# Performance work log

Hardware: AMD Instinct MI355X
Metric: run time of the kernel (lower is better)

The kernel has to match this reference:

```python
import jax, jax.numpy as jnp
import numpy as np
import math

D_MODEL = 2048
N_HEADS = 16
HEAD_DIM = D_MODEL // N_HEADS  # 128
SEQ = 2048
BATCH = 1


def make_freqs(seq_len, head_dim, theta=10000.0):
    # standard rotary frequencies: freqs_cis = exp(i * t * inv_freq)
    inv_freq = 1.0 / (theta ** (np.arange(0, head_dim, 2, dtype=np.float32) / head_dim))
    t = np.arange(seq_len, dtype=np.float32)
    ang = np.outer(t, inv_freq)  # [seq, head_dim/2]
    return jnp.asarray(np.cos(ang)), jnp.asarray(np.sin(ang))


def setup_inputs() -> dict:
    key = jax.random.key(0)
    ks = jax.random.split(key, 6)
    x = jax.random.normal(ks[0], (BATCH, SEQ, D_MODEL), dtype=jnp.float32)
    freqs_cos, freqs_sin = make_freqs(SEQ, HEAD_DIM)
    # causal additive mask, broadcastable to [b, h, s, s]
    mask = jnp.where(jnp.tril(jnp.ones((SEQ, SEQ), dtype=bool)), 0.0, -1e9).astype(jnp.float32)[None, None]
    scale = 0.02
    wq = jax.random.normal(ks[1], (D_MODEL, D_MODEL), dtype=jnp.float32) * scale
    wk = jax.random.normal(ks[2], (D_MODEL, D_MODEL), dtype=jnp.float32) * scale
    wv = jax.random.normal(ks[3], (D_MODEL, D_MODEL), dtype=jnp.float32) * scale
    wo = jax.random.normal(ks[4], (D_MODEL, D_MODEL), dtype=jnp.float32) * scale
    return {"x": x, "freqs_cos": freqs_cos, "freqs_sin": freqs_sin, "mask": mask,
            "wq": wq, "wk": wk, "wv": wv, "wo": wo}


def _apply_rotary(q, k, cos, sin):
    # q, k: [b, s, h, hd]; cos/sin: [s, hd/2]
    def rot(t):
        tr = t.reshape(*t.shape[:-1], -1, 2)  # [b, s, h, hd/2, 2]
        re, im = tr[..., 0], tr[..., 1]
        c = cos[None, :, None, :]
        s = sin[None, :, None, :]
        # complex multiply (re + i im) * (c + i s)
        out_re = re * c - im * s
        out_im = re * s + im * c
        return jnp.stack([out_re, out_im], axis=-1).reshape(t.shape)
    return rot(q), rot(k)


def reference(x, freqs_cos, freqs_sin, mask, wq, wk, wv, wo):
    b, s, _ = x.shape
    # QKV projections (nn.Linear with no bias: x @ W^T; W is square so use x @ W
    # with W stored already-transposed -- weights here are random so x @ W is faithful math)
    q = (x @ wq).reshape(b, s, N_HEADS, HEAD_DIM)
    k = (x @ wk).reshape(b, s, N_HEADS, HEAD_DIM)
    v = (x @ wv).reshape(b, s, N_HEADS, HEAD_DIM)
    q, k = _apply_rotary(q, k, freqs_cos, freqs_sin)
    # [b, h, s_q, s_k]
    scores = jnp.einsum("bqhd,bkhd->bhqk", q, k) / math.sqrt(HEAD_DIM)
    scores = scores + mask
    probs = jax.nn.softmax(scores.astype(jnp.float32), axis=-1).astype(q.dtype)
    out = jnp.einsum("bhqk,bkhd->bqhd", probs, v).reshape(b, s, N_HEADS * HEAD_DIM)
    return out @ wo
```

## Files before the change

### kernel.cpp

```cpp
#include <hip/hip_runtime.h>
#include <hip/hip_bf16.h>
#include <math.h>

#define SEQ 2048
#define DM 2048
#define NH 16
#define HD 128
#define QKV_N 6144

typedef __bf16 bf16;
typedef __bf16 bf16x8 __attribute__((ext_vector_type(8)));
typedef __bf16 bf16x4v __attribute__((ext_vector_type(4)));
typedef __bf16 bf16x2v __attribute__((ext_vector_type(2)));
typedef float f32x4 __attribute__((ext_vector_type(4)));

__device__ inline int sw_idx64(int row, int chunk) {
    return (row * 8 + (chunk ^ (row & 7))) * 8;
}
__device__ inline int sw_idx128(int row, int chunk) {
    return (row * 16 + (chunk ^ (row & 15))) * 8;
}

__device__ inline void async16(const void* g, void* l) {
    __builtin_amdgcn_global_load_lds((const __attribute__((address_space(1))) void*)g,
                                     (__attribute__((address_space(3))) void*)l, 16, 0, 0);
}

__global__ __launch_bounds__(256) void k_prep(const float* __restrict__ wq,
                                              const float* __restrict__ wk,
                                              const float* __restrict__ wv,
                                              const float* __restrict__ wo,
                                              bf16* __restrict__ wT, bf16* __restrict__ woT,
                                              const float* __restrict__ x,
                                              bf16* __restrict__ xb) {
    const int z = blockIdx.z;
    const int t = threadIdx.x;
    if (z == 4) {
        int bid = blockIdx.y * 32 + blockIdx.x;
#pragma unroll
        for (int j = 0; j < 4; ++j) {
            int i = bid * 1024 + j * 256 + t;
            float4 v = ((const float4*)x)[i];
            bf16x4v o;
            o.x = (bf16)v.x; o.y = (bf16)v.y; o.z = (bf16)v.z; o.w = (bf16)v.w;
            ((bf16x4v*)xb)[i] = o;
        }
        return;
    }
    __shared__ bf16 tile[64][66];
    const float* src = (z == 0) ? wq : (z == 1) ? wk : (z == 2) ? wv : wo;
    bf16* dst = (z < 3) ? (wT + (size_t)z * DM * DM) : woT;
    const int bx = blockIdx.x * 64, by = blockIdx.y * 64;
#pragma unroll
    for (int j = 0; j < 4; ++j) {
        int idx = j * 256 + t;
        int r = idx >> 4, cg = idx & 15;
        float4 v = *(const float4*)&src[(size_t)(by + r) * DM + bx + cg * 4];
        bf16x4v o;
        o.x = (bf16)v.x; o.y = (bf16)v.y; o.z = (bf16)v.z; o.w = (bf16)v.w;
        *(bf16x4v*)&tile[r][cg * 4] = o;
    }
    __syncthreads();
#pragma unroll
    for (int j = 0; j < 4; ++j) {
        int idx = j * 256 + t;
        int r = idx >> 4, cg = idx & 15;
        bf16x4v o;
        o.x = tile[cg * 4 + 0][r];
        o.y = tile[cg * 4 + 1][r];
        o.z = tile[cg * 4 + 2][r];
        o.w = tile[cg * 4 + 3][r];
        *(bf16x4v*)&dst[(size_t)(bx + r) * DM + by + cg * 4] = o;
    }
}

__global__ __launch_bounds__(1024) void k_rope(bf16* __restrict__ qkv,
                                               const float* __restrict__ cosT,
                                               const float* __restrict__ sinT) {
    int idx = blockIdx.x * 1024 + threadIdx.x;
    int i = idx & 63;
    int h = (idx >> 6) & 15;
    int s = idx >> 10;
    float c = cosT[s * 64 + i], sn = sinT[s * 64 + i];
    size_t base = (size_t)s * QKV_N + h * HD + 2 * i;
    bf16x2v q = *(bf16x2v*)&qkv[base];
    float qr = (float)q.x, qi = (float)q.y;
    bf16x2v qo;
    qo.x = (bf16)(qr * c - qi * sn);
    qo.y = (bf16)(qr * sn + qi * c);
    *(bf16x2v*)&qkv[base] = qo;
    bf16x2v k = *(bf16x2v*)&qkv[base + DM];
    float kr = (float)k.x, ki = (float)k.y;
    bf16x2v ko;
    ko.x = (bf16)(kr * c - ki * sn);
    ko.y = (bf16)(kr * sn + ki * c);
    *(bf16x2v*)&qkv[base + DM] = ko;
}

__global__ __launch_bounds__(256) void k_vt(const bf16* __restrict__ qkv,
                                            bf16* __restrict__ vT) {
    __shared__ bf16 tile[64][66];
    const int t = threadIdx.x;
    const int bx = blockIdx.x * 64, by = blockIdx.y * 64;
#pragma unroll
    for (int j = 0; j < 4; ++j) {
        int idx = j * 256 + t;
        int r = idx >> 4, cg = idx & 15;
        *(bf16x4v*)&tile[r][cg * 4] =
            *(const bf16x4v*)&qkv[(size_t)(by + r) * QKV_N + 2 * DM + bx + cg * 4];
    }
    __syncthreads();
#pragma unroll
    for (int j = 0; j < 4; ++j) {
        int idx = j * 256 + t;
        int r = idx >> 4, cg = idx & 15;
        bf16x4v o;
        o.x = tile[cg * 4 + 0][r];
        o.y = tile[cg * 4 + 1][r];
        o.z = tile[cg * 4 + 2][r];
        o.w = tile[cg * 4 + 3][r];
        *(bf16x4v*)&vT[(size_t)(bx + r) * SEQ + by + cg * 4] = o;
    }
}

template <typename OutT, int BN>
__device__ __forceinline__ void gemm_body(const bf16* __restrict__ A,
                                          const bf16* __restrict__ Bt,
                                          OutT* __restrict__ C,
                                          int N, int K, size_t bm, size_t bn,
                                          bf16* As, bf16* Bs) {
    constexpr int NI = BN / 32;
    const int t = threadIdx.x;
    const int lane = t & 63;
    const int w = t >> 6;
    const int wr = (w >> 1) * 64, wc = (w & 1) * (BN / 2);
    const int l15 = lane & 15, quad = lane >> 4;
    f32x4 acc[4][NI];
#pragma unroll
    for (int i = 0; i < 4; ++i)
#pragma unroll
        for (int j = 0; j < NI; ++j) acc[i][j] = (f32x4){0.f, 0.f, 0.f, 0.f};

    for (int kt = 0; kt < K; kt += 64) {
#pragma unroll
        for (int j = 0; j < 4; ++j) {
            int c = j * 256 + t;
            int row = c >> 3, g = ((c & 7) ^ (row & 7)) * 8;
            async16(&A[(bm + row) * K + kt + g], &As[c * 8]);
        }
#pragma unroll
        for (int j = 0; j < NI; ++j) {
            int c = j * 256 + t;
            int row = c >> 3, g = ((c & 7) ^ (row & 7)) * 8;
            async16(&Bt[(bn + row) * K + kt + g], &Bs[c * 8]);
        }
        __syncthreads();
#pragma unroll
        for (int kh = 0; kh < 2; ++kh) {
            bf16x8 af[4], bfm[NI];
#pragma unroll
            for (int mi = 0; mi < 4; ++mi)
                af[mi] = *(const bf16x8*)&As[sw_idx64(wr + mi * 16 + l15, kh * 4 + quad)];
#pragma unroll
            for (int ni = 0; ni < NI; ++ni)
                bfm[ni] = *(const bf16x8*)&Bs[sw_idx64(wc + ni * 16 + l15, kh * 4 + quad)];
#pragma unroll
            for (int mi = 0; mi < 4; ++mi)
#pragma unroll
                for (int ni = 0; ni < NI; ++ni)
                    acc[mi][ni] = __builtin_amdgcn_mfma_f32_16x16x32_bf16(
                        af[mi], bfm[ni], acc[mi][ni], 0, 0, 0);
        }
        __syncthreads();
    }
#pragma unroll
    for (int mi = 0; mi < 4; ++mi)
#pragma unroll
        for (int ni = 0; ni < NI; ++ni)
#pragma unroll
            for (int r = 0; r < 4; ++r) {
                size_t row = bm + wr + mi * 16 + quad * 4 + r;
                size_t col = bn + wc + ni * 16 + l15;
                C[row * (size_t)N + col] = (OutT)acc[mi][ni][r];
            }
}

template <typename OutT, int BN>
__global__ __launch_bounds__(256) void k_gemm_bt(const bf16* __restrict__ A,
                                                 const bf16* __restrict__ Bt,
                                                 OutT* __restrict__ C,
                                                 int M, int N, int K) {
    __shared__ bf16 As[128 * 64];
    __shared__ bf16 Bs[BN * 64];
    size_t bm = (size_t)blockIdx.y * 128, bn = (size_t)blockIdx.x * BN;
    gemm_body<OutT, BN>(A, Bt, C, N, K, bm, bn, As, Bs);
}

__global__ __launch_bounds__(256) void k_flash(const bf16* __restrict__ qkv,
                                               const bf16* __restrict__ vT,
                                               bf16* __restrict__ out) {
    __shared__ bf16 Ks[2][64 * 128];
    __shared__ bf16 Vs[2][128 * 64];
    __shared__ bf16 Pl[4][16 * 64];
    const int t = threadIdx.x;
    const int lane = t & 63;
    const int w = t >> 6;
    const int l15 = lane & 15, quad = lane >> 4;
    const int b = blockIdx.x;
    const int h = (b & 7) * 2 + ((b >> 3) & 1);
    const int qb = 31 - (b >> 4);
    const int q0w = qb * 64 + w * 16;
    const float sc2 = 0.08838834764831845f * 1.4426950408889634f;

    const size_t qrow = (size_t)(q0w + l15) * QKV_N + h * HD;
    bf16x8 aq[4];
#pragma unroll
    for (int u = 0; u < 4; ++u)
        aq[u] = *(const bf16x8*)&qkv[qrow + u * 32 + quad * 8];

    f32x4 o[8];
#pragma unroll
    for (int c = 0; c < 8; ++c) o[c] = (f32x4){0.f, 0.f, 0.f, 0.f};
    float l_r[4] = {0.f, 0.f, 0.f, 0.f};

    int krow[4], kg[4], vrow[4], vg[4];
#pragma unroll
    for (int j = 0; j < 4; ++j) {
        int c = j * 256 + t;
        krow[j] = c >> 4; kg[j] = ((c & 15) ^ (krow[j] & 15)) * 8;
        vrow[j] = c >> 3; vg[j] = ((c & 7) ^ (vrow[j] & 7)) * 8;
    }
    auto stage = [&](int buf, int kt2) {
        const int kb2 = kt2 * 64;
#pragma unroll
        for (int j = 0; j < 4; ++j)
            async16(&qkv[(size_t)(kb2 + krow[j]) * QKV_N + DM + h * HD + kg[j]],
                    &Ks[buf][(j * 256 + t) * 8]);
#pragma unroll
        for (int j = 0; j < 4; ++j)
            async16(&vT[(size_t)(h * HD + vrow[j]) * SEQ + kb2 + vg[j]],
                    &Vs[buf][(j * 256 + t) * 8]);
    };

    const int n64 = qb + 1;
    stage(0, 0);
    for (int kt = 0; kt < n64; ++kt) {
        const int cb = kt & 1;
        const int kbase = kt * 64;
        if (kt + 1 < n64) {
            stage(cb ^ 1, kt + 1);
            asm volatile("s_waitcnt vmcnt(8)" ::: "memory");
        } else {
            asm volatile("s_waitcnt vmcnt(0)" ::: "memory");
        }
        __builtin_amdgcn_s_barrier();
        asm volatile("" ::: "memory");

        f32x4 s4[4];
#pragma unroll
        for (int sub = 0; sub < 4; ++sub) {
            f32x4 z = (f32x4){0.f, 0.f, 0.f, 0.f};
#pragma unroll
            for (int u = 0; u < 4; ++u) {
                bf16x8 kv = *(const bf16x8*)&Ks[cb][sw_idx128(sub * 16 + l15, u * 4 + quad)];
                z = __builtin_amdgcn_mfma_f32_16x16x32_bf16(aq[u], kv, z, 0, 0, 0);
            }
            s4[sub] = z;
        }
        const bool masked = (kt == n64 - 1);
#pragma unroll
        for (int sub = 0; sub < 4; ++sub)
#pragma unroll
            for (int r = 0; r < 4; ++r) {
                float p = exp2f(s4[sub][r] * sc2);
                if (masked)
                    p = (kbase + sub * 16 + l15 <= q0w + quad * 4 + r) ? p : 0.f;
                l_r[r] += p;
                int rowp = quad * 4 + r;
                int col = sub * 16 + l15;
                Pl[w][(rowp * 8 + ((col >> 3) ^ (rowp & 7))) * 8 + (col & 7)] = (bf16)p;
            }
        __asm__ __volatile__("s_waitcnt lgkmcnt(0)" ::: "memory");
        bf16x8 pf[2];
#pragma unroll
        for (int kk = 0; kk < 2; ++kk)
            pf[kk] = *(const bf16x8*)&Pl[w][sw_idx64(l15, kk * 4 + quad)];
        __builtin_amdgcn_s_setprio(1);
#pragma unroll
        for (int c = 0; c < 8; ++c)
#pragma unroll
            for (int kk = 0; kk < 2; ++kk) {
                bf16x8 vb = *(const bf16x8*)&Vs[cb][sw_idx64(c * 16 + l15, kk * 4 + quad)];
                o[c] = __builtin_amdgcn_mfma_f32_16x16x32_bf16(pf[kk], vb, o[c], 0, 0, 0);
            }
        __builtin_amdgcn_s_setprio(0);
        asm volatile("" ::: "memory");
        __builtin_amdgcn_s_barrier();
        asm volatile("" ::: "memory");
    }

    float rl[4];
#pragma unroll
    for (int r = 0; r < 4; ++r) {
        float l = l_r[r];
        l += __shfl_xor(l, 1, 16);
        l += __shfl_xor(l, 2, 16);
        l += __shfl_xor(l, 4, 16);
        l += __shfl_xor(l, 8, 16);
        rl[r] = 1.0f / l;
    }
#pragma unroll
    for (int c = 0; c < 8; ++c)
#pragma unroll
        for (int r = 0; r < 4; ++r)
            out[(size_t)(q0w + quad * 4 + r) * DM + h * HD + c * 16 + l15] =
                (bf16)(o[c][r] * rl[r]);
}

extern "C" void kernel_launch(void* const* d_in, const int* in_sizes, int n_in,
                              void* d_out, int out_size, void* d_ws, size_t ws_size,
                              hipStream_t stream) {
    const float* x  = (const float*)d_in[0];
    const float* fc = (const float*)d_in[1];
    const float* fs = (const float*)d_in[2];
    const float* wq = (const float*)d_in[4];
    const float* wk = (const float*)d_in[5];
    const float* wv = (const float*)d_in[6];
    const float* wo = (const float*)d_in[7];
    float* out = (float*)d_out;

    char* ws = (char*)d_ws;
    bf16* xb  = (bf16*)(ws);
    bf16* wT  = (bf16*)(ws + (size_t)(8u  << 20));
    bf16* woT = (bf16*)(ws + (size_t)(32u << 20));
    bf16* qkv = (bf16*)(ws + (size_t)(40u << 20));
    bf16* vT  = (bf16*)(ws + (size_t)(64u << 20));

    k_prep<<<dim3(32, 32, 5), 256, 0, stream>>>(wq, wk, wv, wo, wT, woT, x, xb);
    k_gemm_bt<bf16, 128><<<dim3(48, 16), 256, 0, stream>>>(xb, wT, qkv, SEQ, QKV_N, DM);
    k_rope<<<2048, 1024, 0, stream>>>(qkv, fc, fs);
    k_vt<<<dim3(32, 32), 256, 0, stream>>>(qkv, vT);
    k_flash<<<512, 256, 0, stream>>>(qkv, vT, xb);
    k_gemm_bt<float, 128><<<dim3(16, 16), 256, 0, stream>>>(xb, woT, out, SEQ, DM, DM);
}
```

Measured before the change: 304.9 us.

## Fuse K-rope with V transpose, apply Q rope inside flash, retile output GEMM

Merges the rope and V-transpose kernels into one launch, with the first 1024 blocks doing the transpose and the remaining blocks applying rotary to K using 16-byte vector accesses. Rotary for Q is moved into the flash attention kernel, applied to the Q fragments in registers right after loading, so Q is never rewritten to memory. The output projection GEMM switches to BN=64 tiles to launch twice as many blocks. This removes one kernel launch and a read-modify-write pass over Q, at the cost of extra cos/sin loads in flash and smaller per-block reuse in the output GEMM.

```diff
diff --git a/kernel.cpp b/kernel.cpp
--- a/kernel.cpp
+++ b/kernel.cpp
@@ -74,34 +74,34 @@
     }
 }
 
-__global__ __launch_bounds__(1024) void k_rope(bf16* __restrict__ qkv,
-                                               const float* __restrict__ cosT,
-                                               const float* __restrict__ sinT) {
-    int idx = blockIdx.x * 1024 + threadIdx.x;
-    int i = idx & 63;
-    int h = (idx >> 6) & 15;
-    int s = idx >> 10;
-    float c = cosT[s * 64 + i], sn = sinT[s * 64 + i];
-    size_t base = (size_t)s * QKV_N + h * HD + 2 * i;
-    bf16x2v q = *(bf16x2v*)&qkv[base];
-    float qr = (float)q.x, qi = (float)q.y;
-    bf16x2v qo;
-    qo.x = (bf16)(qr * c - qi * sn);
-    qo.y = (bf16)(qr * sn + qi * c);
-    *(bf16x2v*)&qkv[base] = qo;
-    bf16x2v k = *(bf16x2v*)&qkv[base + DM];
-    float kr = (float)k.x, ki = (float)k.y;
-    bf16x2v ko;
-    ko.x = (bf16)(kr * c - ki * sn);
-    ko.y = (bf16)(kr * sn + ki * c);
-    *(bf16x2v*)&qkv[base + DM] = ko;
-}
-
-__global__ __launch_bounds__(256) void k_vt(const bf16* __restrict__ qkv,
-                                            bf16* __restrict__ vT) {
+__global__ __launch_bounds__(256) void k_rope_vt(bf16* __restrict__ qkv,
+                                                 const float* __restrict__ cosT,
+                                                 const float* __restrict__ sinT,
+                                                 bf16* __restrict__ vT) {
+    const int t = threadIdx.x;
+    if (blockIdx.x >= 1024) {
+        int g = (blockIdx.x - 1024) * 256 + t;
+        int s = g >> 8;
+        int cg = g & 255;
+        int h = cg >> 4, w8 = cg & 15;
+        size_t base = (size_t)s * QKV_N + DM + h * HD + w8 * 8;
+        float4 cv = *(const float4*)&cosT[s * 64 + w8 * 4];
+        float4 sv = *(const float4*)&sinT[s * 64 + w8 * 4];
+        float cc[4] = {cv.x, cv.y, cv.z, cv.w};
+        float ss[4] = {sv.x, sv.y, sv.z, sv.w};
+        bf16x8 k = *(bf16x8*)&qkv[base];
+        bf16x8 o;
+#pragma unroll
+        for (int p = 0; p < 4; ++p) {
+            float re = (float)k[2 * p], im = (float)k[2 * p + 1];
+            o[2 * p]     = (bf16)(re * cc[p] - im * ss[p]);
+            o[2 * p + 1] = (bf16)(re * ss[p] + im * cc[p]);
+        }
+        *(bf16x8*)&qkv[base] = o;
+        return;
+    }
     __shared__ bf16 tile[64][66];
-    const int t = threadIdx.x;
-    const int bx = blockIdx.x * 64, by = blockIdx.y * 64;
+    const int bx = (blockIdx.x & 31) * 64, by = (blockIdx.x >> 5) * 64;
 #pragma unroll
     for (int j = 0; j < 4; ++j) {
         int idx = j * 256 + t;
@@ -198,6 +198,8 @@
 
 __global__ __launch_bounds__(256) void k_flash(const bf16* __restrict__ qkv,
                                                const bf16* __restrict__ vT,
+                                               const float* __restrict__ cosT,
+                                               const float* __restrict__ sinT,
                                                bf16* __restrict__ out) {
     __shared__ bf16 Ks[2][64 * 128];
     __shared__ bf16 Vs[2][128 * 64];
@@ -217,6 +219,21 @@
 #pragma unroll
     for (int u = 0; u < 4; ++u)
         aq[u] = *(const bf16x8*)&qkv[qrow + u * 32 + quad * 8];
+#pragma unroll
+    for (int u = 0; u < 4; ++u) {
+        float4 cv = *(const float4*)&cosT[(q0w + l15) * 64 + u * 16 + quad * 4];
+        float4 sv = *(const float4*)&sinT[(q0w + l15) * 64 + u * 16 + quad * 4];
+        float cc[4] = {cv.x, cv.y, cv.z, cv.w};
+        float ss[4] = {sv.x, sv.y, sv.z, sv.w};
+        bf16x8 q = aq[u], rq;
+#pragma unroll
+        for (int p = 0; p < 4; ++p) {
+            float re = (float)q[2 * p], im = (float)q[2 * p + 1];
+            rq[2 * p]     = (bf16)(re * cc[p] - im * ss[p]);
+            rq[2 * p + 1] = (bf16)(re * ss[p] + im * cc[p]);
+        }
+        aq[u] = rq;
+    }
 
     f32x4 o[8];
 #pragma unroll
@@ -338,8 +355,7 @@
 
     k_prep<<<dim3(32, 32, 5), 256, 0, stream>>>(wq, wk, wv, wo, wT, woT, x, xb);
     k_gemm_bt<bf16, 128><<<dim3(48, 16), 256, 0, stream>>>(xb, wT, qkv, SEQ, QKV_N, DM);
-    k_rope<<<2048, 1024, 0, stream>>>(qkv, fc, fs);
-    k_vt<<<dim3(32, 32), 256, 0, stream>>>(qkv, vT);
-    k_flash<<<512, 256, 0, stream>>>(qkv, vT, xb);
-    k_gemm_bt<float, 128><<<dim3(16, 16), 256, 0, stream>>>(xb, woT, out, SEQ, DM, DM);
-}
+    k_rope_vt<<<3072, 256, 0, stream>>>(qkv, fc, fs, vT);
+    k_flash<<<512, 256, 0, stream>>>(qkv, vT, fc, fs, xb);
+    k_gemm_bt<float, 64><<<dim3(32, 16), 256, 0, stream>>>(xb, woT, out, SEQ, DM, DM);
+}
```

Measured after the change: 293.0 us. 3.9% less time.
